# Performance work log

Hardware: AMD Instinct MI355X
Metric: run time of the kernel (lower is better)

The kernel has to match this reference:

```python
import jax, jax.numpy as jnp
import numpy as np

EPS_NORM = 1e-12   # torch F.normalize eps
GN_EPS = 1e-5      # GroupNorm eps
FACTOR = 5
NUM_HEADS = 8
NEG_SLOPE = 0.01   # LeakyReLU default


def _l2norm(x, axis):
    n = jnp.sqrt(jnp.sum(x * x, axis=axis, keepdims=True))
    return x / jnp.maximum(n, EPS_NORM)


def setup_inputs() -> dict:
    key = jax.random.key(0)
    B, C, H, W, D = 2, 256, 16, 16, 16
    N = H * W * D
    sample_k = FACTOR * int(np.ceil(np.log(N)))  # 45
    ks = jax.random.split(key, 8)
    s = 0.02
    return {
        "x": jax.random.normal(ks[0], (B, C, H, W, D), jnp.float32),
        "W_qkvv": jax.random.normal(ks[1], (C, 4 * C), jnp.float32) * s,
        "W_out": jax.random.normal(ks[2], (C, C), jnp.float32) * s,
        "b_out": jnp.zeros((C,), jnp.float32),
        "W_out2": jax.random.normal(ks[3], (C, C), jnp.float32) * s,
        "b_out2": jnp.zeros((C,), jnp.float32),
        "gamma1": 0.1 * jnp.ones((C,), jnp.float32),
        "conv_w": jax.random.normal(ks[4], (C, C, 3, 3, 3), jnp.float32) * s,
        "gn_w": jnp.ones((C,), jnp.float32),
        "gn_b": jnp.zeros((C,), jnp.float32),
        "index_sample": jax.random.randint(ks[5], (N, sample_k), 0, N),
    }


def reference(x, W_qkvv, W_out, b_out, W_out2, b_out2, gamma1, conv_w, gn_w, gn_b, index_sample):
    B, C, H, Wd, D = x.shape
    N = H * Wd * D
    nh = NUM_HEADS
    dh = C // nh
    xs = x.reshape(B, C, N).transpose(0, 2, 1)                    # [B,N,C]
    qkvv = (xs @ W_qkvv).reshape(B, N, 4, nh, dh).transpose(2, 0, 3, 1, 4)  # [4,B,nh,N,dh]
    q, k, v_ca, v_sa = qkvv[0], qkvv[1], qkvv[2], qkvv[3]
    q = _l2norm(q, axis=-2)   # normalize over sequence dim (dim=-2 in torch)
    k = _l2norm(k, axis=-2)

    u = FACTOR * int(np.ceil(np.log(N)))
    # --- ProbSparse _prob_QK ---
    K_sample = k[:, :, index_sample, :]                            # [B,nh,N,sk,dh]
    QK_sample = jnp.einsum('bhle,bhlse->bhls', q, K_sample)        # [B,nh,N,sk]
    M = QK_sample.max(-1) - QK_sample.sum(-1) / N                  # sparsity measure
    _, M_top = jax.lax.top_k(M, u)                                 # [B,nh,u]
    b_idx = jnp.arange(B)[:, None, None]
    h_idx = jnp.arange(nh)[None, :, None]
    Q_red = q[b_idx, h_idx, M_top]                                 # [B,nh,u,dh]
    scores = jnp.einsum('bhud,bhld->bhul', Q_red, k)               # [B,nh,u,N]

    # --- spatial (ProbSparse) context ---
    ctx = jnp.broadcast_to(v_sa.mean(axis=-2, keepdims=True), v_sa.shape)  # [B,nh,N,dh]
    attn_sa = jax.nn.softmax(scores, axis=-1)
    upd = jnp.einsum('bhul,bhld->bhud', attn_sa, v_sa)             # [B,nh,u,dh]
    ctx = ctx.at[b_idx, h_idx, M_top].set(upd)

    # --- channel attention (on transposed q,k,v: [B,nh,dh,N]) ---
    qt = q.transpose(0, 1, 3, 2)
    kt = k.transpose(0, 1, 3, 2)
    vt = v_ca.transpose(0, 1, 3, 2)
    attn_ca = jax.nn.softmax(jnp.einsum('bhdn,bhen->bhde', qt, kt), axis=-1)  # [B,nh,dh,dh]
    x_ca = jnp.einsum('bhde,bhen->bhdn', attn_ca, vt).transpose(0, 3, 1, 2).reshape(B, N, C)
    x_sa = ctx.transpose(0, 3, 1, 2).reshape(B, N, C)              # matches source permute
    x_sa = x_sa @ W_out + b_out                                    # dead branch (source discards)
    x_ca = x_ca @ W_out2 + b_out2
    epa = x_ca  # source: x = x_SA + x_CA; x = x_CA  -> only CA branch survives

    attn = xs + gamma1 * epa                                       # [B,N,C]
    attn = attn.reshape(B, H, Wd, D, C).transpose(0, 4, 1, 2, 3)   # [B,C,H,W,D]

    # conv8: Dropout3d (eval=id) -> Conv3d(3x3x3, no bias) -> GroupNorm(1 group)
    y = jax.lax.conv_general_dilated(attn, conv_w, (1, 1, 1), [(1, 1)] * 3,
                                     dimension_numbers=('NCDHW', 'OIDHW', 'NCDHW'))
    mu = y.mean(axis=(1, 2, 3, 4), keepdims=True)
    var = y.var(axis=(1, 2, 3, 4), keepdims=True)
    y = (y - mu) / jnp.sqrt(var + GN_EPS)
    y = y * gn_w[None, :, None, None, None] + gn_b[None, :, None, None, None]
    y = y + attn
    return jnp.where(y >= 0, y, NEG_SLOPE * y)
```

## Files before the change

### kernel.cpp

```cpp
#include <hip/hip_runtime.h>
#include <hip/hip_bf16.h>
#include <stdint.h>


#define B_ 2
#define C_ 256
#define N_ 4096
#define NH 8
#define PADV 5832
#define CN  (C_*N_)
#define BCN (B_*CN)

typedef unsigned short u16;
typedef unsigned int   u32;

using frag16 = __attribute__((ext_vector_type(8))) short;
using f32x4  = __attribute__((ext_vector_type(4))) float;

__device__ __forceinline__ u16 f2bf(float f) {
    u32 u = __float_as_uint(f);
    u += 0x7fff + ((u >> 16) & 1);
    return (u16)(u >> 16);
}
__device__ __forceinline__ float bb(u16 h) { return __uint_as_float((u32)h << 16); }
__device__ __forceinline__ void gld16(const void* g, void* l) {
    __builtin_amdgcn_global_load_lds((const __attribute__((address_space(1))) u32*)g,
                                     (__attribute__((address_space(3))) u32*)l, 16, 0, 0);
}
__device__ __forceinline__ int padrow(int n) {
    int z = n >> 8, y = (n >> 4) & 15, x = n & 15;
    return (z + 1) * 324 + (y + 1) * 18 + (x + 1);
}

#define OFF_XB16  0
#define OFF_GP    1048576
#define OFF_NQK   2097152
#define OFF_PK    0
#define OFF_Y     3145728
#define OFF_ATTB  4194304
#define OFF_ATTP  5242880
#define OFF_WT2   6735872
#define OFF_W2B   7620608
#define OFF_WQB   7653376
#define OFF_XT    7751680
#define OFF_WVT   8800256
#define OFF_MT    8898560
#define OFF_WFU   8964096
#define OFF_NRM   9029632
#define OFF_RED   9030656

__global__ __launch_bounds__(256) void k_prep(const float* __restrict__ CW, const float* __restrict__ W2,
                                              const float* __restrict__ Wq, const float* __restrict__ X,
                                              u16* __restrict__ WT2, u16* __restrict__ W2B,
                                              u16* __restrict__ Wqb, u16* __restrict__ WvT,
                                              u16* __restrict__ XT, u16* __restrict__ XB,
                                              u32* __restrict__ APz, float* __restrict__ NRM) {
    __shared__ __align__(16) float ls[6912];
    float (*ts)[33] = (float(*)[33])ls;
    float (*t64)[65] = (float(*)[65])ls;
    int blk = blockIdx.x, tid = threadIdx.x;
    if (blk < 256) {
        int co = blk;
        const float* src = CW + (size_t)co * 6912;
        for (int u = tid; u < 6912; u += 256) ls[u] = src[u];
        __syncthreads();
#pragma unroll
        for (int t = 0; t < 27; ++t)
            WT2[(((size_t)t * 256 + co) << 8) + tid] = f2bf(ls[tid * 27 + t]);
    } else if (blk < 320) {
        int bi = blk - 256; int c0 = (bi & 7) * 32, p0 = (bi >> 3) * 32;
        int tx = tid & 31, ty = tid >> 5;
#pragma unroll
        for (int i = 0; i < 4; ++i) ts[ty + i * 8][tx] = W2[(size_t)(p0 + ty + i * 8) * 256 + c0 + tx];
        __syncthreads();
#pragma unroll
        for (int i = 0; i < 4; ++i) W2B[(size_t)(c0 + ty + i * 8) * 256 + p0 + tx] = f2bf(ts[tx][ty + i * 8]);
    } else if (blk < 512) {
        int bi = blk - 320; int c0 = (bi & 7) * 32, j0 = (bi >> 3) * 32;
        int tx = tid & 31, ty = tid >> 5;
#pragma unroll
        for (int i = 0; i < 4; ++i) ts[ty + i * 8][tx] = Wq[(size_t)(c0 + ty + i * 8) * 1024 + j0 + tx];
        __syncthreads();
#pragma unroll
        for (int i = 0; i < 4; ++i) Wqb[(size_t)(j0 + ty + i * 8) * 256 + c0 + tx] = f2bf(ts[tx][ty + i * 8]);
    } else if (blk < 768) {
        int c = blk - 512;
        WvT[(size_t)c * 256 + tid] = f2bf(Wq[(size_t)c * 1024 + 512 + tid]);
    } else if (blk < 1280) {
        int idx = blk - 768;
        int n0 = (idx & 63) * 64, c0 = ((idx >> 6) & 3) * 64, b = idx >> 8;
        int tn = tid & 63, tc4 = tid >> 6;
        const float* Xb = X + (size_t)b * CN;
        u16* XBb = XB + (size_t)b * CN;
#pragma unroll
        for (int i = 0; i < 16; ++i) {
            int c = c0 + tc4 + i * 4;
            float v = Xb[(size_t)c * N_ + n0 + tn];
            t64[tc4 + i * 4][tn] = v;
            XBb[(size_t)c * N_ + n0 + tn] = f2bf(v);
        }
        __syncthreads();
        u16* Xo = XT + (size_t)b * N_ * C_;
#pragma unroll
        for (int i = 0; i < 16; ++i)
            Xo[(size_t)(n0 + tc4 + i * 4) * C_ + c0 + tn] = f2bf(t64[tn][tc4 + i * 4]);
    } else if (blk < 7112) {
        APz[(size_t)(blk - 1280) * 256 + tid] = 0;
    } else {
        ((float4*)NRM)[tid] = make_float4(0.f, 0.f, 0.f, 0.f);
    }
}

__global__ __launch_bounds__(256) void k_gram(const u16* __restrict__ XB, float* __restrict__ GP) {
    __shared__ __align__(16) u16 As[2][8192], Bs[2][8192];
    int mt = blockIdx.x & 1, nt = blockIdx.x >> 1, s = blockIdx.y, b = blockIdx.z;
    int c0 = mt * 128, c0p = nt * 128, k0 = s * 512;
    int tid = threadIdx.x, lane = tid & 63, w = tid >> 6;
    int wm = w & 1, wn = w >> 1, qm = lane >> 4, lm = lane & 15;
    int srow = lane >> 3;
    int sperm = (((lane & 7) ^ srow) << 3);
    const u16* aB = XB + ((size_t)(b * 256 + c0 + w * 32 + srow)) * 4096 + k0 + sperm;
    const u16* bB = XB + ((size_t)(b * 256 + c0p + w * 32 + srow)) * 4096 + k0 + sperm;
    int rdp = ((lm & 7) << 3);
    f32x4 acc[4][4] = {};
    auto stg = [&](int p, int kt) {
#pragma unroll
        for (int i = 0; i < 4; ++i) {
            gld16(aB + (size_t)i * 32768 + kt * 64, &As[p][w * 2048 + i * 512]);
            gld16(bB + (size_t)i * 32768 + kt * 64, &Bs[p][w * 2048 + i * 512]);
        }
    };
    stg(0, 0);
#pragma unroll
    for (int kt = 0; kt < 8; ++kt) {
        int p = kt & 1;
        __syncthreads();
        if (kt < 7) stg(p ^ 1, kt + 1);
#pragma unroll
        for (int c2 = 0; c2 < 2; ++c2) {
            frag16 af[4], bf[4];
#pragma unroll
            for (int i = 0; i < 4; ++i)
                af[i] = *(const frag16*)&As[p][(wm * 64 + i * 16 + lm) * 64 + ((((c2 * 4 + qm) << 3) ^ rdp))];
#pragma unroll
            for (int j = 0; j < 4; ++j)
                bf[j] = *(const frag16*)&Bs[p][(wn * 64 + j * 16 + lm) * 64 + ((((c2 * 4 + qm) << 3) ^ rdp))];
#pragma unroll
            for (int i = 0; i < 4; ++i)
#pragma unroll
                for (int j = 0; j < 4; ++j)
                    acc[i][j] = __builtin_amdgcn_mfma_f32_16x16x32_bf16(af[i], bf[j], acc[i][j], 0, 0, 0);
        }
    }
    float* o = GP + (((size_t)s * B_ + b) * 256 + c0 + wm * 64) * 256 + c0p + wn * 64;
#pragma unroll
    for (int i = 0; i < 4; ++i)
#pragma unroll
        for (int j = 0; j < 4; ++j)
#pragma unroll
            for (int r = 0; r < 4; ++r)
                o[(size_t)(i * 16 + qm * 4 + r) * 256 + j * 16 + lm] = acc[i][j][r];
}

__global__ __launch_bounds__(256) void k_nqk(const float* __restrict__ GP, const u16* __restrict__ Wqb,
                                             u16* __restrict__ NQK, float* __restrict__ NRM) {
    __shared__ float Gs[16][260];
    int ct = blockIdx.x, h = blockIdx.y, b = blockIdx.z, t = threadIdx.x;
#pragma unroll
    for (int i = 0; i < 16; ++i) {
        float v = 0.f;
#pragma unroll
        for (int s = 0; s < 8; ++s)
            v += GP[(((size_t)s * B_ + b) * 256 + ct * 16 + i) * 256 + t];
        Gs[i][t] = v;
    }
    __syncthreads();
    int o = t >> 3, cg = t & 7;
    int cl0 = cg * 2, cl1 = cg * 2 + 1;
    const u16* Wk = Wqb + (size_t)(256 + h * 32 + o) * 256;
    const u16* Wqr = Wqb + (size_t)(h * 32 + o) * 256;
    float ak0 = 0.f, ak1 = 0.f, aq0 = 0.f, aq1 = 0.f;
    for (int cp = 0; cp < 256; cp += 8) {
        uint4 kv = *(const uint4*)(Wk + cp);
        uint4 qv = *(const uint4*)(Wqr + cp);
        const u16 *kh = (const u16*)&kv, *qh = (const u16*)&qv;
#pragma unroll
        for (int j = 0; j < 8; ++j) {
            float kf = bb(kh[j]), qf = bb(qh[j]);
            float g0 = Gs[cl0][cp + j], g1v = Gs[cl1][cp + j];
            ak0 += kf * g0; ak1 += kf * g1v;
            aq0 += qf * g0; aq1 += qf * g1v;
        }
    }
    size_t base_q = (((size_t)(b * NH + h) * 2 + 0) * 32 + o) * 256 + ct * 16 + cg * 2;
    *(u32*)(NQK + base_q)        = (u32)f2bf(aq0) | ((u32)f2bf(aq1) << 16);
    *(u32*)(NQK + base_q + 8192) = (u32)f2bf(ak0) | ((u32)f2bf(ak1) << 16);
    u32 wq = *(const u32*)(Wqr + ct * 16 + cg * 2);
    u32 wk = *(const u32*)(Wk + ct * 16 + cg * 2);
    float pq = bb((u16)wq) * aq0 + bb((u16)(wq >> 16)) * aq1;
    float pk = bb((u16)wk) * ak0 + bb((u16)(wk >> 16)) * ak1;
    pq += __shfl_xor(pq, 1); pq += __shfl_xor(pq, 2); pq += __shfl_xor(pq, 4);
    pk += __shfl_xor(pk, 1); pk += __shfl_xor(pk, 2); pk += __shfl_xor(pk, 4);
    if (cg == 0) {
        atomicAdd(&NRM[b * 512 + h * 64 + o], pq);
        atomicAdd(&NRM[b * 512 + h * 64 + 32 + o], pk);
    }
}

__global__ __launch_bounds__(256) void k_soft(const u16* __restrict__ NQK, const u16* __restrict__ Wqb,
                                              const u16* __restrict__ WvT, const float* __restrict__ NRM,
                                              u16* __restrict__ MT) {
    __shared__ __align__(16) u16 Ws[8192], Ns[8192];
    __shared__ float Sm[32][33];
    __shared__ float Ab[32][33];
    __shared__ float iqS[32], ikS[32];
    int h = blockIdx.x, b = blockIdx.y;
    int tid = threadIdx.x, lane = tid & 63, w = tid >> 6;
    int wm = w & 1, wn = w >> 1, qm = lane >> 4, lm = lane & 15;
    const u16* Wq = Wqb + ((size_t)h * 32) * 256;
    const u16* NK = NQK + (((size_t)(b * NH + h) * 2 + 1) * 32) * 256;
#pragma unroll
    for (int rp = 0; rp < 4; ++rp) {
        int row = rp * 8 + w * 2 + (lane >> 5);
        int cg = (lane & 31) ^ (row & 31);
        gld16(Wq + (size_t)row * 256 + cg * 8, &Ws[rp * 2048 + w * 512]);
        gld16(NK + (size_t)row * 256 + cg * 8, &Ns[rp * 2048 + w * 512]);
    }
    if (tid < 32) {
        iqS[tid] = 1.0f / fmaxf(sqrtf(fmaxf(NRM[b * 512 + h * 64 + tid], 0.f)), 1e-12f);
        ikS[tid] = 1.0f / fmaxf(sqrtf(fmaxf(NRM[b * 512 + h * 64 + 32 + tid], 0.f)), 1e-12f);
    }
    __syncthreads();
    f32x4 acc = {};
    int rowA = wm * 16 + lm, rowB = wn * 16 + lm;
#pragma unroll
    for (int kk = 0; kk < 8; ++kk) {
        int sA = ((kk * 4 + qm) ^ (rowA & 31)) << 3;
        int sB = ((kk * 4 + qm) ^ (rowB & 31)) << 3;
        frag16 af = *(const frag16*)&Ws[rowA * 256 + sA];
        frag16 bf = *(const frag16*)&Ns[rowB * 256 + sB];
        acc = __builtin_amdgcn_mfma_f32_16x16x32_bf16(af, bf, acc, 0, 0, 0);
    }
#pragma unroll
    for (int r = 0; r < 4; ++r) Sm[wm * 16 + qm * 4 + r][wn * 16 + lm] = acc[r];
    __syncthreads();
    if (tid < 32) {
        float iq = iqS[tid];
        float sv[32], m = -1e30f;
#pragma unroll
        for (int e = 0; e < 32; ++e) { sv[e] = Sm[tid][e] * iq * ikS[e]; m = fmaxf(m, sv[e]); }
        float sm = 0.f;
#pragma unroll
        for (int e = 0; e < 32; ++e) { sv[e] = __expf(sv[e] - m); sm += sv[e]; }
        float rin = 1.0f / sm;
#pragma unroll
        for (int e = 0; e < 32; ++e) Ab[tid][e] = sv[e] * rin;
    }
    __syncthreads();
    frag16 bf2[2];
#pragma unroll
    for (int j = 0; j < 2; ++j) {
        __align__(16) u16 tmp[8];
#pragma unroll
        for (int ii = 0; ii < 8; ++ii) tmp[ii] = f2bf(Ab[j * 16 + lm][qm * 8 + ii]);
        bf2[j] = *(const frag16*)tmp;
    }
    f32x4 acc2[4][2] = {};
#pragma unroll
    for (int i = 0; i < 4; ++i) {
        int row = w * 64 + i * 16 + lm;
        frag16 af = *(const frag16*)&WvT[(size_t)row * 256 + h * 32 + qm * 8];
#pragma unroll
        for (int j = 0; j < 2; ++j)
            acc2[i][j] = __builtin_amdgcn_mfma_f32_16x16x32_bf16(af, bf2[j], acc2[i][j], 0, 0, 0);
    }
    u16* Mo = MT + (size_t)b * 65536;
#pragma unroll
    for (int i = 0; i < 4; ++i)
#pragma unroll
        for (int j = 0; j < 2; ++j)
#pragma unroll
            for (int r = 0; r < 4; ++r)
                Mo[(size_t)(w * 64 + i * 16 + qm * 4 + r) * 256 + h * 32 + j * 16 + lm] = f2bf(acc2[i][j][r]);
}

__global__ __launch_bounds__(256) void k_wfull(const u16* __restrict__ W2B, const u16* __restrict__ MT,
                                               const float* __restrict__ g1, u16* __restrict__ WFU) {
    __shared__ __align__(16) u16 As[2][8192], Bs[2][8192];
    int c0 = blockIdx.x * 128, cq0 = blockIdx.y * 128, b = blockIdx.z;
    int tid = threadIdx.x, lane = tid & 63, w = tid >> 6;
    int wm = w & 1, wn = w >> 1, qm = lane >> 4, lm = lane & 15;
    int srow = lane >> 3;
    int sperm = (((lane & 7) ^ srow) << 3);
    const u16* aB = W2B + ((size_t)(c0 + w * 32 + srow)) * 256 + sperm;
    const u16* bB = MT + ((size_t)(b * 256 + cq0 + w * 32 + srow)) * 256 + sperm;
    int rdp = ((lm & 7) << 3);
    f32x4 acc[4][4] = {};
    auto stg = [&](int p, int kc) {
#pragma unroll
        for (int i = 0; i < 4; ++i) {
            gld16(aB + i * 2048 + kc * 64, &As[p][w * 2048 + i * 512]);
            gld16(bB + i * 2048 + kc * 64, &Bs[p][w * 2048 + i * 512]);
        }
    };
    stg(0, 0);
#pragma unroll
    for (int kt = 0; kt < 4; ++kt) {
        int p = kt & 1;
        __syncthreads();
        if (kt < 3) stg(p ^ 1, kt + 1);
#pragma unroll
        for (int c2 = 0; c2 < 2; ++c2) {
            frag16 af[4], bf[4];
#pragma unroll
            for (int i = 0; i < 4; ++i)
                af[i] = *(const frag16*)&As[p][(wm * 64 + i * 16 + lm) * 64 + ((((c2 * 4 + qm) << 3) ^ rdp))];
#pragma unroll
            for (int j = 0; j < 4; ++j)
                bf[j] = *(const frag16*)&Bs[p][(wn * 64 + j * 16 + lm) * 64 + ((((c2 * 4 + qm) << 3) ^ rdp))];
#pragma unroll
            for (int i = 0; i < 4; ++i)
#pragma unroll
                for (int j = 0; j < 4; ++j)
                    acc[i][j] = __builtin_amdgcn_mfma_f32_16x16x32_bf16(af[i], bf[j], acc[i][j], 0, 0, 0);
        }
    }
#pragma unroll
    for (int i = 0; i < 4; ++i)
#pragma unroll
        for (int r = 0; r < 4; ++r) {
            int c = c0 + wm * 64 + i * 16 + qm * 4 + r;
            float gv = g1[c];
#pragma unroll
            for (int j = 0; j < 4; ++j) {
                int cc = cq0 + wn * 64 + j * 16 + lm;
                WFU[((size_t)b * 256 + c) * 256 + cc] = f2bf(gv * acc[i][j][r]);
            }
        }
}

__global__ __launch_bounds__(256) void k_att(const u16* __restrict__ WFU, const u16* __restrict__ XT,
                                             const float* __restrict__ bias2, const float* __restrict__ g1,
                                             const float* __restrict__ X, u16* __restrict__ ATTb,
                                             u16* __restrict__ ATTp) {
    __shared__ __align__(16) u16 As[2][8192], Bs[2][8192];
    int n0 = blockIdx.x * 128, c0 = blockIdx.y * 128, b = blockIdx.z;
    int tid = threadIdx.x, lane = tid & 63, w = tid >> 6;
    int wm = w & 1, wn = w >> 1, qm = lane >> 4, lm = lane & 15;
    int srow = lane >> 3;
    int sperm = (((lane & 7) ^ srow) << 3);
    const u16* aB = WFU + ((size_t)(b * 256 + c0 + w * 32 + srow)) * 256 + sperm;
    const u16* bB = XT + ((size_t)(b * N_ + n0 + w * 32 + srow)) * 256 + sperm;
    int rdp = ((lm & 7) << 3);
    f32x4 acc[4][4] = {};
    auto stg = [&](int p, int kc) {
#pragma unroll
        for (int i = 0; i < 4; ++i) {
            gld16(aB + i * 2048 + kc * 64, &As[p][w * 2048 + i * 512]);
            gld16(bB + i * 2048 + kc * 64, &Bs[p][w * 2048 + i * 512]);
        }
    };
    stg(0, 0);
#pragma unroll
    for (int kt = 0; kt < 4; ++kt) {
        int p = kt & 1;
        __syncthreads();
        if (kt < 3) stg(p ^ 1, kt + 1);
#pragma unroll
        for (int c2 = 0; c2 < 2; ++c2) {
            frag16 af[4], bf[4];
#pragma unroll
            for (int i = 0; i < 4; ++i)
                af[i] = *(const frag16*)&As[p][(wm * 64 + i * 16 + lm) * 64 + ((((c2 * 4 + qm) << 3) ^ rdp))];
#pragma unroll
            for (int j = 0; j < 4; ++j)
                bf[j] = *(const frag16*)&Bs[p][(wn * 64 + j * 16 + lm) * 64 + ((((c2 * 4 + qm) << 3) ^ rdp))];
#pragma unroll
            for (int i = 0; i < 4; ++i)
#pragma unroll
                for (int j = 0; j < 4; ++j)
                    acc[i][j] = __builtin_amdgcn_mfma_f32_16x16x32_bf16(af[i], bf[j], acc[i][j], 0, 0, 0);
        }
    }
    int c_base = c0 + wm * 64, n_base = n0 + wn * 64;
    const float* xin = X + (size_t)b * CN;
    u16* Ao = ATTb + (size_t)b * CN;
    u16* Ap = ATTp + ((size_t)b * PADV << 8);
    float val[4][4][4];
#pragma unroll
    for (int i = 0; i < 4; ++i)
#pragma unroll
        for (int r = 0; r < 4; ++r) {
            int c = c_base + i * 16 + qm * 4 + r;
            float gb2 = g1[c] * bias2[c];
#pragma unroll
            for (int j = 0; j < 4; ++j) {
                int n = n_base + j * 16 + lm;
                float v = xin[(size_t)c * N_ + n] + acc[i][j][r] + gb2;
                val[i][j][r] = v;
                Ao[(size_t)c * N_ + n] = f2bf(v);
            }
        }
#pragma unroll
    for (int j = 0; j < 4; ++j) {
        int n = n_base + j * 16 + lm;
        int pr = padrow(n);
#pragma unroll
        for (int i = 0; i < 4; ++i) {
            ushort4 pk;
            pk.x = f2bf(val[i][j][0]); pk.y = f2bf(val[i][j][1]);
            pk.z = f2bf(val[i][j][2]); pk.w = f2bf(val[i][j][3]);
            *(ushort4*)&Ap[((size_t)pr << 8) + c_base + i * 16 + qm * 4] = pk;
        }
    }
}

__global__ __launch_bounds__(256) void k_conv_mfma(const u16* __restrict__ WT2, const u16* __restrict__ ATTp,
                                                   u16* __restrict__ Pk) {
    __shared__ __align__(16) u16 As[2][8192], Bs[2][4096];
    int n0 = blockIdx.x * 64;
    int co0 = (blockIdx.y & 1) * 128, ks = blockIdx.y >> 1;
    int b = blockIdx.z;
    int tid = threadIdx.x, lane = tid & 63, w = tid >> 6;
    int wm = w & 1, wn = w >> 1, qm = lane >> 4, lm = lane & 15;
    int srow = lane >> 3;
    int sperm = (((lane & 7) ^ srow) << 3);
    const u16* aB = WT2 + (((size_t)ks * 9 * 256 + co0 + w * 32 + srow) << 8) + sperm;
    int prA[2];
#pragma unroll
    for (int i = 0; i < 2; ++i) prA[i] = padrow(n0 + w * 16 + i * 8 + srow) << 8;
    const u16* bB = ATTp + ((size_t)b * PADV << 8) + ((ks - 1) * 324 << 8) + sperm;
    int rdp = ((lm & 7) << 3);
    f32x4 acc[4][2] = {};
    auto stg = [&](int p, int kt) {
        int tap9 = kt >> 2, kc = kt & 3;
        int K9 = ((tap9 / 3) - 1) * 18 + (tap9 % 3 - 1);
#pragma unroll
        for (int i = 0; i < 4; ++i)
            gld16(aB + (size_t)tap9 * 65536 + i * 2048 + kc * 64, &As[p][w * 2048 + i * 512]);
#pragma unroll
        for (int i = 0; i < 2; ++i)
            gld16(bB + prA[i] + K9 * 256 + kc * 64, &Bs[p][w * 1024 + i * 512]);
    };
    stg(0, 0);
#pragma unroll
    for (int kt = 0; kt < 36; ++kt) {
        int p = kt & 1;
        __syncthreads();
        if (kt < 35) stg(p ^ 1, kt + 1);
#pragma unroll
        for (int c2 = 0; c2 < 2; ++c2) {
            frag16 af[4], bf[2];
#pragma unroll
            for (int i = 0; i < 4; ++i)
                af[i] = *(const frag16*)&As[p][(wm * 64 + i * 16 + lm) * 64 + ((((c2 * 4 + qm) << 3) ^ rdp))];
#pragma unroll
            for (int j = 0; j < 2; ++j)
                bf[j] = *(const frag16*)&Bs[p][(wn * 32 + j * 16 + lm) * 64 + ((((c2 * 4 + qm) << 3) ^ rdp))];
#pragma unroll
            for (int i = 0; i < 4; ++i)
#pragma unroll
                for (int j = 0; j < 2; ++j)
                    acc[i][j] = __builtin_amdgcn_mfma_f32_16x16x32_bf16(af[i], bf[j], acc[i][j], 0, 0, 0);
        }
    }
    u16* Pb = Pk + ((size_t)(ks * B_ + b) * C_ + co0 + wm * 64) * N_ + n0 + wn * 32;
#pragma unroll
    for (int i = 0; i < 4; ++i)
#pragma unroll
        for (int j = 0; j < 2; ++j)
#pragma unroll
            for (int r = 0; r < 4; ++r)
                Pb[(size_t)(i * 16 + qm * 4 + r) * N_ + j * 16 + lm] = f2bf(acc[i][j][r]);
}

__global__ __launch_bounds__(256) void k_gn_reduce(const u16* __restrict__ Pk, u16* __restrict__ Y,
                                                   float* __restrict__ RED) {
    int blk = blockIdx.x, b = blockIdx.y;
    size_t base = (size_t)b * CN + (size_t)blk * 16384;
    const u16* p0 = Pk + base;
    const u16* p1 = Pk + BCN + base;
    const u16* p2 = Pk + (size_t)2 * BCN + base;
    u16* y = Y + base;
    float s = 0.f, q = 0.f;
    for (int u = threadIdx.x * 8; u < 16384; u += 2048) {
        uint4 a = *(const uint4*)&p0[u];
        uint4 c1 = *(const uint4*)&p1[u];
        uint4 c2 = *(const uint4*)&p2[u];
        const u16 *A = (const u16*)&a, *B1 = (const u16*)&c1, *C2 = (const u16*)&c2;
        __align__(16) u16 outp[8];
#pragma unroll
        for (int i = 0; i < 8; ++i) {
            float v = bb(A[i]) + bb(B1[i]) + bb(C2[i]);
            s += v; q += v * v;
            outp[i] = f2bf(v);
        }
        *(uint4*)&y[u] = *(const uint4*)outp;
    }
#pragma unroll
    for (int off = 32; off; off >>= 1) { s += __shfl_down(s, off); q += __shfl_down(q, off); }
    __shared__ float rs_[4], rq[4];
    int lane = threadIdx.x & 63, wv = threadIdx.x >> 6;
    if (!lane) { rs_[wv] = s; rq[wv] = q; }
    __syncthreads();
    if (threadIdx.x == 0) {
        RED[((size_t)b * 64 + blk) * 2 + 0] = rs_[0] + rs_[1] + rs_[2] + rs_[3];
        RED[((size_t)b * 64 + blk) * 2 + 1] = rq[0] + rq[1] + rq[2] + rq[3];
    }
}

__global__ __launch_bounds__(256) void k_final(const u16* __restrict__ Y, const u16* __restrict__ ATTb,
                                               const float* __restrict__ RED, const float* __restrict__ gw,
                                               const float* __restrict__ gb, float* __restrict__ out) {
    int i = blockIdx.x * 256 + threadIdx.x;
    int b = i >> 20;
    int c = (i >> 12) & 255;
    __shared__ float smu[2];
    if (threadIdx.x < 64) {
        float s = RED[((size_t)b * 64 + threadIdx.x) * 2 + 0];
        float q = RED[((size_t)b * 64 + threadIdx.x) * 2 + 1];
#pragma unroll
        for (int off = 32; off; off >>= 1) { s += __shfl_down(s, off); q += __shfl_down(q, off); }
        if (threadIdx.x == 0) {
            float inv = 1.0f / (float)CN;
            float mu = s * inv, var = q * inv - mu * mu;
            smu[0] = mu; smu[1] = rsqrtf(var + 1e-5f);
        }
    }
    __syncthreads();
    float v = (bb(Y[i]) - smu[0]) * smu[1] * gw[c] + gb[c] + bb(ATTb[i]);
    out[i] = v >= 0.f ? v : 0.01f * v;
}

extern "C" void kernel_launch(void* const* d_in, const int* in_sizes, int n_in,
                              void* d_out, int out_size, void* d_ws, size_t ws_size,
                              hipStream_t stream) {
    const float* x      = (const float*)d_in[0];
    const float* Wqkvv  = (const float*)d_in[1];
    const float* W_out2 = (const float*)d_in[4];
    const float* b_out2 = (const float*)d_in[5];
    const float* gamma1 = (const float*)d_in[6];
    const float* conv_w = (const float*)d_in[7];
    const float* gn_w   = (const float*)d_in[8];
    const float* gn_b   = (const float*)d_in[9];
    float* out = (float*)d_out;
    float* ws = (float*)d_ws;

    u16*   XB   = (u16*)(ws + OFF_XB16);
    float* GP   = ws + OFF_GP;
    u16*   NQK  = (u16*)(ws + OFF_NQK);
    u16*   Pk   = (u16*)(ws + OFF_PK);
    u16*   Y    = (u16*)(ws + OFF_Y);
    u16*   ATTb = (u16*)(ws + OFF_ATTB);
    u16*   ATTp = (u16*)(ws + OFF_ATTP);
    u16*   WT2  = (u16*)(ws + OFF_WT2);
    u16*   W2B  = (u16*)(ws + OFF_W2B);
    u16*   Wqb  = (u16*)(ws + OFF_WQB);
    u16*   XT   = (u16*)(ws + OFF_XT);
    u16*   WvT  = (u16*)(ws + OFF_WVT);
    u16*   MT   = (u16*)(ws + OFF_MT);
    u16*   WFU  = (u16*)(ws + OFF_WFU);
    float* NRM  = ws + OFF_NRM;
    float* RED  = ws + OFF_RED;

    k_prep      <<<7113, 256, 0, stream>>>(conv_w, W_out2, Wqkvv, x, WT2, W2B, Wqb, WvT, XT, XB, (u32*)ATTp, NRM);
    k_gram      <<<dim3(4, 8, B_), 256, 0, stream>>>(XB, GP);
    k_nqk       <<<dim3(16, NH, B_), 256, 0, stream>>>(GP, Wqb, NQK, NRM);
    k_soft      <<<dim3(NH, B_), 256, 0, stream>>>(NQK, Wqb, WvT, NRM, MT);
    k_wfull     <<<dim3(2, 2, B_), 256, 0, stream>>>(W2B, MT, gamma1, WFU);
    k_att       <<<dim3(32, 2, B_), 256, 0, stream>>>(WFU, XT, b_out2, gamma1, x, ATTb, ATTp);
    k_conv_mfma <<<dim3(64, 6, B_), 256, 0, stream>>>(WT2, ATTp, Pk);
    k_gn_reduce <<<dim3(64, B_), 256, 0, stream>>>(Pk, Y, RED);
    k_final     <<<8192, 256, 0, stream>>>(Y, ATTb, RED, gn_w, gn_b, out);
}
```

Before: 182.4 us.

## Load conv weight fragments directly from global into registers, bypassing LDS

```diff
diff --git a/kernel.cpp b/kernel.cpp
--- a/kernel.cpp
+++ b/kernel.cpp
@@ -417,7 +417,7 @@
 
 __global__ __launch_bounds__(256) void k_conv_mfma(const u16* __restrict__ WT2, const u16* __restrict__ ATTp,
                                                    u16* __restrict__ Pk) {
-    __shared__ __align__(16) u16 As[2][8192], Bs[2][4096];
+    __shared__ __align__(16) u16 Bs[2][4096];
     int n0 = blockIdx.x * 64;
     int co0 = (blockIdx.y & 1) * 128, ks = blockIdx.y >> 1;
     int b = blockIdx.z;
@@ -425,35 +425,43 @@
     int wm = w & 1, wn = w >> 1, qm = lane >> 4, lm = lane & 15;
     int srow = lane >> 3;
     int sperm = (((lane & 7) ^ srow) << 3);
-    const u16* aB = WT2 + (((size_t)ks * 9 * 256 + co0 + w * 32 + srow) << 8) + sperm;
+    const u16* aRow[4];
+#pragma unroll
+    for (int i = 0; i < 4; ++i)
+        aRow[i] = WT2 + (((size_t)ks * 9 * 256 + co0 + wm * 64 + i * 16 + lm) << 8);
     int prA[2];
 #pragma unroll
     for (int i = 0; i < 2; ++i) prA[i] = padrow(n0 + w * 16 + i * 8 + srow) << 8;
     const u16* bB = ATTp + ((size_t)b * PADV << 8) + ((ks - 1) * 324 << 8) + sperm;
     int rdp = ((lm & 7) << 3);
     f32x4 acc[4][2] = {};
-    auto stg = [&](int p, int kt) {
+    auto stgB = [&](int p, int kt) {
         int tap9 = kt >> 2, kc = kt & 3;
         int K9 = ((tap9 / 3) - 1) * 18 + (tap9 % 3 - 1);
-#pragma unroll
-        for (int i = 0; i < 4; ++i)
-            gld16(aB + (size_t)tap9 * 65536 + i * 2048 + kc * 64, &As[p][w * 2048 + i * 512]);
 #pragma unroll
         for (int i = 0; i < 2; ++i)
             gld16(bB + prA[i] + K9 * 256 + kc * 64, &Bs[p][w * 1024 + i * 512]);
     };
-    stg(0, 0);
+    auto ldA = [&](int kt, int c2, frag16* af) {
+        int tap9 = kt >> 2, kc = kt & 3;
+        size_t off = ((size_t)tap9 << 16) + kc * 64 + (c2 * 4 + qm) * 8;
+#pragma unroll
+        for (int i = 0; i < 4; ++i) af[i] = *(const frag16*)(aRow[i] + off);
+    };
+    stgB(0, 0);
+    frag16 afc[4];
+    ldA(0, 0, afc);
 #pragma unroll
     for (int kt = 0; kt < 36; ++kt) {
         int p = kt & 1;
         __syncthreads();
-        if (kt < 35) stg(p ^ 1, kt + 1);
+        if (kt < 35) stgB(p ^ 1, kt + 1);
 #pragma unroll
         for (int c2 = 0; c2 < 2; ++c2) {
-            frag16 af[4], bf[2];
-#pragma unroll
-            for (int i = 0; i < 4; ++i)
-                af[i] = *(const frag16*)&As[p][(wm * 64 + i * 16 + lm) * 64 + ((((c2 * 4 + qm) << 3) ^ rdp))];
+            frag16 afn[4];
+            if (c2 == 0) ldA(kt, 1, afn);
+            else ldA(kt < 35 ? kt + 1 : kt, 0, afn);
+            frag16 bf[2];
 #pragma unroll
             for (int j = 0; j < 2; ++j)
                 bf[j] = *(const frag16*)&Bs[p][(wn * 32 + j * 16 + lm) * 64 + ((((c2 * 4 + qm) << 3) ^ rdp))];
@@ -461,7 +469,9 @@
             for (int i = 0; i < 4; ++i)
 #pragma unroll
                 for (int j = 0; j < 2; ++j)
-                    acc[i][j] = __builtin_amdgcn_mfma_f32_16x16x32_bf16(af[i], bf[j], acc[i][j], 0, 0, 0);
+                    acc[i][j] = __builtin_amdgcn_mfma_f32_16x16x32_bf16(afc[i], bf[j], acc[i][j], 0, 0, 0);
+#pragma unroll
+            for (int i = 0; i < 4; ++i) afc[i] = afn[i];
         }
     }
     u16* Pb = Pk + ((size_t)(ks * B_ + b) * C_ + co0 + wm * 64) * N_ + n0 + wn * 32;
```

Result: slower. 246.8 us (+35.3%).
